# Optimization experiments

Measured on AMD Instinct MI355X. Metric: run time of the kernel, lower is better.

Reference implementation:

```python
import jax, jax.numpy as jnp
import numpy as np

N_NODES = 100000
N_EDGES = 1600000
K = 5  # TAGConv hops
F_IN, F_HID, F_OUT = 64, 128, 64


def setup_inputs() -> dict:
    key = jax.random.key(0)
    ks = jax.random.split(key, 6)
    x = jax.random.normal(ks[0], (N_NODES, F_IN), dtype=jnp.float32)
    edge_index = jax.random.randint(ks[1], (2, N_EDGES), 0, N_NODES, dtype=jnp.int32)
    edge_weight = jax.random.uniform(ks[2], (N_EDGES,), dtype=jnp.float32)
    # TAGConv layer l has (K+1) weight matrices stacked as [K+1, in, out] + one bias
    W0 = jax.random.normal(ks[3], (K + 1, F_IN, F_HID), dtype=jnp.float32) * 0.05
    b0 = jnp.zeros((F_HID,), dtype=jnp.float32)
    W1 = jax.random.normal(ks[4], (K + 1, F_HID, F_OUT), dtype=jnp.float32) * 0.05
    b1 = jnp.zeros((F_OUT,), dtype=jnp.float32)
    return {"x": x, "edge_index": edge_index, "edge_weight": edge_weight,
            "W0": W0, "b0": b0, "W1": W1, "b1": b1}


def _gcn_norm(edge_weight, row, col):
    # symmetric normalization, no added self-loops (TAGConv default with edge_weight)
    deg = jax.ops.segment_sum(edge_weight, col, num_segments=N_NODES)
    safe_deg = jnp.where(deg > 0, deg, 1.0)
    dis = jnp.where(deg > 0, jax.lax.rsqrt(safe_deg), 0.0)  # deg^-1/2, 0 for isolated
    return dis[row] * edge_weight * dis[col]


def _tag_conv(x, row, col, norm, W, b):
    # out = sum_{k=0..K} (A_norm^k x) @ W[k] + b
    out = x @ W[0]
    h = x
    for k in range(1, K + 1):
        msg = h[row] * norm[:, None]                    # gather + scale  [E, F]
        h = jax.ops.segment_sum(msg, col, num_segments=N_NODES)  # scatter-add [N, F]
        out = out + h @ W[k]
    return out + b


def reference(x, edge_index, edge_weight, W0, b0, W1, b1):
    row, col = edge_index[0], edge_index[1]
    norm = _gcn_norm(edge_weight, row, col)
    h = jax.nn.leaky_relu(_tag_conv(x, row, col, norm, W0, b0), negative_slope=0.01)
    h = jax.nn.leaky_relu(_tag_conv(h, row, col, norm, W1, b1), negative_slope=0.01)
    return h
```

## Files before the change

### kernel.cpp

```cpp
#include <hip/hip_runtime.h>


namespace {
constexpr int NN = 100000;
constexpr int NE = 1600000;
constexpr int TPB = 256;

typedef __attribute__((ext_vector_type(8))) short short8v;
typedef __attribute__((ext_vector_type(4))) float float4v;

__device__ __forceinline__ float bflo(unsigned p) { return __uint_as_float(p << 16); }
__device__ __forceinline__ float bfhi(unsigned p) { return __uint_as_float(p & 0xffff0000u); }
__device__ __forceinline__ unsigned f2bf(float x) {
  unsigned u = __float_as_uint(x);
  return (u + 0x7fffu + ((u >> 16) & 1u)) >> 16;
}
__device__ __forceinline__ unsigned pack2(float lo, float hi) {
  return f2bf(lo) | (f2bf(hi) << 16);
}

__global__ void pass1_kernel(const int* __restrict__ col, const float* __restrict__ w,
                             unsigned* __restrict__ acc32, int* __restrict__ rank) {
  int e = blockIdx.x * TPB + threadIdx.x;
  if (e >= NE) return;
  int c = col[e];
  unsigned v = (1u << 21) | (unsigned)__float2uint_rn(w[e] * 8192.0f);
  unsigned old = atomicAdd(&acc32[c], v);
  rank[e] = (int)(old >> 21);
}

__global__ void dis_kernel(const unsigned* __restrict__ acc32, float* __restrict__ dis) {
  int n = blockIdx.x * TPB + threadIdx.x;
  if (n >= NN) return;
  float d = (float)(acc32[n] & 0x1FFFFFu) * (1.0f / 8192.0f);
  dis[n] = d > 0.f ? rsqrtf(d) : 0.f;
}

__global__ void scan1_kernel(const unsigned* __restrict__ acc32, int* __restrict__ excl,
                             int* __restrict__ btot) {
  __shared__ int sh[1024];
  int i = blockIdx.x * 1024 + threadIdx.x;
  int v = (i < NN) ? (int)(acc32[i] >> 21) : 0;
  sh[threadIdx.x] = v;
  __syncthreads();
  for (int ofs = 1; ofs < 1024; ofs <<= 1) {
    int t = (threadIdx.x >= ofs) ? sh[threadIdx.x - ofs] : 0;
    __syncthreads();
    sh[threadIdx.x] += t;
    __syncthreads();
  }
  if (i < NN) excl[i] = sh[threadIdx.x] - v;
  if (threadIdx.x == 1023) btot[blockIdx.x] = sh[1023];
}

__global__ void scan2_kernel(int* __restrict__ btot, int nb) {
  __shared__ int sh[128];
  int t = threadIdx.x;
  if (t < nb) sh[t] = btot[t];
  __syncthreads();
  if (t == 0) {
    int run = 0;
    for (int b = 0; b < nb; ++b) { int x = sh[b]; sh[b] = run; run += x; }
  }
  __syncthreads();
  if (t < nb) btot[t] = sh[t];
}

__global__ void scan3_kernel(const int* __restrict__ excl, const int* __restrict__ btot,
                             int* __restrict__ rowptr) {
  int i = blockIdx.x * TPB + threadIdx.x;
  if (i < NN) rowptr[i] = excl[i] + btot[i >> 10];
  if (i == NN) rowptr[NN] = NE;
}

__global__ void fill2_kernel(const int* __restrict__ row, const int* __restrict__ col,
                             const float* __restrict__ w, const float* __restrict__ dis,
                             const int* __restrict__ rank, const int* __restrict__ rowptr,
                             int2* __restrict__ edges) {
  int e = blockIdx.x * TPB + threadIdx.x;
  if (e >= NE) return;
  int r = row[e], c = col[e];
  float nw = dis[r] * w[e] * dis[c];
  edges[rowptr[c] + rank[e]] = make_int2(r, __float_as_int(nw));
}

__global__ void wfrag0_kernel(const float* __restrict__ W0, short* __restrict__ F) {
  int t = blockIdx.x * TPB + threadIdx.x;
  if (t >= 12 * 8 * 64) return;
  int l = t & 63, nt = (t >> 6) & 7, s = t >> 9;
  int c = nt * 16 + (l & 15);
  int kb = s * 32 + (l >> 4) * 8;
  short8v v;
#pragma unroll
  for (int j = 0; j < 8; ++j) v[j] = (short)f2bf(W0[(kb + j) * 128 + c]);
  *(short8v*)(F + (size_t)t * 8) = v;
}

__global__ void wfrag1_kernel(const float* __restrict__ W1, short* __restrict__ F) {
  int t = blockIdx.x * TPB + threadIdx.x;
  if (t >= 4 * 24 * 64) return;
  int l = t & 63, nt = (t >> 6) % 24, s = t / (64 * 24);
  int J = nt * 16 + (l & 15);
  int fb = s * 32 + (l >> 4) * 8;
  const float* Wb = W1 + (size_t)(J >> 6) * (128 * 64) + (J & 63);
  short8v v;
#pragma unroll
  for (int j = 0; j < 8; ++j) v[j] = (short)f2bf(Wb[(size_t)(fb + j) * 64]);
  *(short8v*)(F + (size_t)t * 8) = v;
}

__global__ void convx_kernel(const float* __restrict__ x, unsigned* __restrict__ hcat) {
  unsigned idx = blockIdx.x * (unsigned)TPB + threadIdx.x;
  if (idx >= (unsigned)NN * 32u) return;
  unsigned n = idx >> 5, p = idx & 31u;
  float2 v = *(const float2*)(x + (size_t)n * 64 + p * 2);
  hcat[(size_t)n * 192 + p] = pack2(v.x, v.y);
}

__device__ __forceinline__ void fma8(float* a, uint4 p, float w) {
  a[0] = fmaf(bflo(p.x), w, a[0]); a[1] = fmaf(bfhi(p.x), w, a[1]);
  a[2] = fmaf(bflo(p.y), w, a[2]); a[3] = fmaf(bfhi(p.y), w, a[3]);
  a[4] = fmaf(bflo(p.z), w, a[4]); a[5] = fmaf(bfhi(p.z), w, a[5]);
  a[6] = fmaf(bflo(p.w), w, a[6]); a[7] = fmaf(bfhi(p.w), w, a[7]);
}

template <bool YADD, bool FINAL>
__global__ void hop_kernel(const unsigned short* __restrict__ src, int sstride,
                           const int2* __restrict__ edges, const int* __restrict__ rowptr,
                           const unsigned short* __restrict__ y,
                           unsigned short* __restrict__ dst, int dstride,
                           const float* __restrict__ bias, float* __restrict__ outf) {
  unsigned n = blockIdx.x * 32u + (threadIdx.x >> 3);
  unsigned lane = threadIdx.x & 7u;
  unsigned f0 = lane * 8u;
  int e = rowptr[n], e1 = rowptr[n + 1];
  float a[8] = {};
  for (; e + 3 < e1; e += 4) {
    int2 d0 = edges[e], d1 = edges[e + 1], d2 = edges[e + 2], d3 = edges[e + 3];
    uint4 p0 = *(const uint4*)(src + (size_t)(unsigned)d0.x * sstride + f0);
    uint4 p1 = *(const uint4*)(src + (size_t)(unsigned)d1.x * sstride + f0);
    uint4 p2 = *(const uint4*)(src + (size_t)(unsigned)d2.x * sstride + f0);
    uint4 p3 = *(const uint4*)(src + (size_t)(unsigned)d3.x * sstride + f0);
    fma8(a, p0, __int_as_float(d0.y));
    fma8(a, p1, __int_as_float(d1.y));
    fma8(a, p2, __int_as_float(d2.y));
    fma8(a, p3, __int_as_float(d3.y));
  }
  if (e + 1 < e1) {
    int2 d0 = edges[e], d1 = edges[e + 1];
    uint4 p0 = *(const uint4*)(src + (size_t)(unsigned)d0.x * sstride + f0);
    uint4 p1 = *(const uint4*)(src + (size_t)(unsigned)d1.x * sstride + f0);
    fma8(a, p0, __int_as_float(d0.y));
    fma8(a, p1, __int_as_float(d1.y));
    e += 2;
  }
  if (e < e1) {
    int2 d0 = edges[e];
    uint4 p0 = *(const uint4*)(src + (size_t)(unsigned)d0.x * sstride + f0);
    fma8(a, p0, __int_as_float(d0.y));
  }
  if (YADD) {
    uint4 yv = *(const uint4*)(y + (size_t)n * 384 + f0);
    a[0] += bflo(yv.x); a[1] += bfhi(yv.x);
    a[2] += bflo(yv.y); a[3] += bfhi(yv.y);
    a[4] += bflo(yv.z); a[5] += bfhi(yv.z);
    a[6] += bflo(yv.w); a[7] += bfhi(yv.w);
  }
  if (FINAL) {
    const float4* bp = (const float4*)(bias + f0);
    float4 bv0 = bp[0], bv1 = bp[1];
    float4 o0, o1;
    o0.x = a[0] + bv0.x; o0.y = a[1] + bv0.y; o0.z = a[2] + bv0.z; o0.w = a[3] + bv0.w;
    o1.x = a[4] + bv1.x; o1.y = a[5] + bv1.y; o1.z = a[6] + bv1.z; o1.w = a[7] + bv1.w;
    o0.x = o0.x >= 0.f ? o0.x : 0.01f * o0.x; o0.y = o0.y >= 0.f ? o0.y : 0.01f * o0.y;
    o0.z = o0.z >= 0.f ? o0.z : 0.01f * o0.z; o0.w = o0.w >= 0.f ? o0.w : 0.01f * o0.w;
    o1.x = o1.x >= 0.f ? o1.x : 0.01f * o1.x; o1.y = o1.y >= 0.f ? o1.y : 0.01f * o1.y;
    o1.z = o1.z >= 0.f ? o1.z : 0.01f * o1.z; o1.w = o1.w >= 0.f ? o1.w : 0.01f * o1.w;
    float4* op = (float4*)(outf + (size_t)n * 64 + f0);
    op[0] = o0; op[1] = o1;
  } else {
    uint4 st;
    st.x = pack2(a[0], a[1]); st.y = pack2(a[2], a[3]);
    st.z = pack2(a[4], a[5]); st.w = pack2(a[6], a[7]);
    *(uint4*)(dst + (size_t)n * dstride + f0) = st;
  }
}

__global__ void gemm_l0(const unsigned short* __restrict__ A, const short* __restrict__ W0f,
                        const float* __restrict__ bias, unsigned short* __restrict__ H1) {
  int wave = threadIdx.x >> 6, lane = threadIdx.x & 63;
  int lrow = lane & 15, lk = lane >> 4;
  unsigned r0 = blockIdx.x * 64u + (unsigned)wave * 16u;
  unsigned arow = r0 + (unsigned)lrow;
  if (arow >= NN) arow = NN - 1;
  const short8v* Ab = (const short8v*)(A + (size_t)arow * 384 + (unsigned)lk * 8);
  const short8v* Bb = (const short8v*)W0f + lane;
  float4v acc[8] = {};
#pragma unroll
  for (int s = 0; s < 12; ++s) {
    short8v a = Ab[s * 4];
#pragma unroll
    for (int nt = 0; nt < 8; ++nt) {
      short8v b = Bb[(s * 8 + nt) * 64];
      acc[nt] = __builtin_amdgcn_mfma_f32_16x16x32_bf16(a, b, acc[nt], 0, 0, 0);
    }
  }
#pragma unroll
  for (int nt = 0; nt < 8; ++nt) {
    int c = nt * 16 + lrow;
    float bv = bias[c];
#pragma unroll
    for (int r = 0; r < 4; ++r) {
      unsigned n = r0 + (unsigned)(lk * 4 + r);
      if (n < NN) {
        float v = acc[nt][r] + bv;
        v = v >= 0.f ? v : 0.01f * v;
        H1[(size_t)n * 128 + c] = (unsigned short)f2bf(v);
      }
    }
  }
}

__global__ void gemm_l1(const unsigned short* __restrict__ A, const short* __restrict__ W1f,
                        unsigned short* __restrict__ Y) {
  int wave = threadIdx.x >> 6, lane = threadIdx.x & 63;
  int lrow = lane & 15, lk = lane >> 4;
  int yb = blockIdx.y * 8;
  unsigned r0 = blockIdx.x * 64u + (unsigned)wave * 16u;
  unsigned arow = r0 + (unsigned)lrow;
  if (arow >= NN) arow = NN - 1;
  const short8v* Ab = (const short8v*)(A + (size_t)arow * 128 + (unsigned)lk * 8);
  const short8v* Bb = (const short8v*)W1f + lane;
  float4v acc[8] = {};
#pragma unroll
  for (int s = 0; s < 4; ++s) {
    short8v a = Ab[s * 4];
#pragma unroll
    for (int nt = 0; nt < 8; ++nt) {
      short8v b = Bb[(s * 24 + yb + nt) * 64];
      acc[nt] = __builtin_amdgcn_mfma_f32_16x16x32_bf16(a, b, acc[nt], 0, 0, 0);
    }
  }
#pragma unroll
  for (int nt = 0; nt < 8; ++nt) {
    int c = (yb + nt) * 16 + lrow;
#pragma unroll
    for (int r = 0; r < 4; ++r) {
      unsigned n = r0 + (unsigned)(lk * 4 + r);
      if (n < NN) Y[(size_t)n * 384 + c] = (unsigned short)f2bf(acc[nt][r]);
    }
  }
}

}

extern "C" void kernel_launch(void* const* d_in, const int* in_sizes, int n_in,
                              void* d_out, int out_size, void* d_ws, size_t ws_size,
                              hipStream_t stream) {
  const float* x  = (const float*)d_in[0];
  const int*   ei = (const int*)d_in[1];
  const float* ew = (const float*)d_in[2];
  const float* W0 = (const float*)d_in[3];
  const float* b0 = (const float*)d_in[4];
  const float* W1 = (const float*)d_in[5];
  const float* b1 = (const float*)d_in[6];
  float* out = (float*)d_out;
  const int* row = ei;
  const int* col = ei + NE;

  constexpr size_t OFF_DIS    = 0;
  constexpr size_t OFF_ROWPTR = 100352;
  constexpr size_t OFF_BTOT   = OFF_ROWPTR + 100352;
  constexpr size_t OFF_EDGES  = OFF_BTOT + 128;
  constexpr size_t OFF_HCAT   = OFF_EDGES + 2 * (size_t)NE;
  constexpr size_t OFF_H1     = OFF_HCAT + (size_t)NN * 384 / 2;
  constexpr size_t WS_WORDS   = OFF_H1 + (size_t)NN * 128 / 2;
  if (ws_size < WS_WORDS * sizeof(float)) return;

  float* ws = (float*)d_ws;
  float* dis    = ws + OFF_DIS;
  int*   rowptr = (int*)(ws + OFF_ROWPTR);
  int*   btot   = (int*)(ws + OFF_BTOT);
  int2*  edges  = (int2*)(ws + OFF_EDGES);
  unsigned short* Hcat = (unsigned short*)(ws + OFF_HCAT);
  unsigned short* H1   = (unsigned short*)(ws + OFF_H1);
  short* W0f = (short*)(ws + OFF_DIS);
  short* W1f = (short*)(ws + OFF_DIS + 24576);
  unsigned* acc32 = (unsigned*)(ws + OFF_H1);
  int* excl = (int*)(ws + OFF_H1 + 100352);
  int* rank = (int*)Hcat;
  unsigned short* z0 = H1;
  unsigned short* z1 = H1 + (size_t)NN * 64;

  hipMemsetAsync(acc32, 0, NN * sizeof(unsigned), stream);
  pass1_kernel<<<(NE + TPB - 1) / TPB, TPB, 0, stream>>>(col, ew, acc32, rank);
  dis_kernel<<<(NN + TPB - 1) / TPB, TPB, 0, stream>>>(acc32, dis);
  scan1_kernel<<<98, 1024, 0, stream>>>(acc32, excl, btot);
  scan2_kernel<<<1, 128, 0, stream>>>(btot, 98);
  scan3_kernel<<<(NN + TPB) / TPB, TPB, 0, stream>>>(excl, btot, rowptr);
  fill2_kernel<<<(NE + TPB - 1) / TPB, TPB, 0, stream>>>(row, col, ew, dis, rank, rowptr, edges);
  wfrag0_kernel<<<24, TPB, 0, stream>>>(W0, W0f);
  wfrag1_kernel<<<24, TPB, 0, stream>>>(W1, W1f);

  convx_kernel<<<NN * 32 / TPB, TPB, 0, stream>>>(x, (unsigned*)Hcat);
  for (int k = 1; k <= 5; ++k) {
    hop_kernel<false, false><<<NN / 32, TPB, 0, stream>>>(
        Hcat + (k - 1) * 64, 384, edges, rowptr, nullptr,
        Hcat + k * 64, 384, nullptr, nullptr);
  }
  gemm_l0<<<(NN + 63) / 64, TPB, 0, stream>>>(Hcat, W0f, b0, H1);

  gemm_l1<<<dim3((NN + 63) / 64, 3), TPB, 0, stream>>>(H1, W1f, Hcat);
  const unsigned short* Y = Hcat;
  hop_kernel<true, false><<<NN / 32, TPB, 0, stream>>>(
      Y + 5 * 64, 384, edges, rowptr, Y + 4 * 64, z0, 64, nullptr, nullptr);
  hop_kernel<true, false><<<NN / 32, TPB, 0, stream>>>(
      z0, 64, edges, rowptr, Y + 3 * 64, z1, 64, nullptr, nullptr);
  hop_kernel<true, false><<<NN / 32, TPB, 0, stream>>>(
      z1, 64, edges, rowptr, Y + 2 * 64, z0, 64, nullptr, nullptr);
  hop_kernel<true, false><<<NN / 32, TPB, 0, stream>>>(
      z0, 64, edges, rowptr, Y + 1 * 64, z1, 64, nullptr, nullptr);
  hop_kernel<true, true><<<NN / 32, TPB, 0, stream>>>(
      z1, 64, edges, rowptr, Y + 0 * 64, nullptr, 0, b1, out);
}
```

Measured before the change: 628.1 us.

## Split node feature matrices into 16-wide column slabs for hop gathers

Node feature buffers are changed from row-major wide rows to four planar slabs of 16 bf16 features per node. Hop kernels launch one grid row per slab, so each gather touches a smaller, denser working set. The GEMM kernels read and write the same slab layout. The trade-off is that the edge list and row pointers are read four times per hop, and each lane issues narrower 4-byte loads.

```diff
diff --git a/kernel.cpp b/kernel.cpp
--- a/kernel.cpp
+++ b/kernel.cpp
@@ -5,6 +5,7 @@
 constexpr int NN = 100000;
 constexpr int NE = 1600000;
 constexpr int TPB = 256;
+constexpr size_t QS = (size_t)NN * 16;
 
 typedef __attribute__((ext_vector_type(8))) short short8v;
 typedef __attribute__((ext_vector_type(4))) float float4v;
@@ -109,80 +110,60 @@
   *(short8v*)(F + (size_t)t * 8) = v;
 }
 
-__global__ void convx_kernel(const float* __restrict__ x, unsigned* __restrict__ hcat) {
+__global__ void convx_kernel(const float* __restrict__ x, unsigned short* __restrict__ hcat) {
   unsigned idx = blockIdx.x * (unsigned)TPB + threadIdx.x;
-  if (idx >= (unsigned)NN * 32u) return;
-  unsigned n = idx >> 5, p = idx & 31u;
-  float2 v = *(const float2*)(x + (size_t)n * 64 + p * 2);
-  hcat[(size_t)n * 192 + p] = pack2(v.x, v.y);
-}
-
-__device__ __forceinline__ void fma8(float* a, uint4 p, float w) {
-  a[0] = fmaf(bflo(p.x), w, a[0]); a[1] = fmaf(bfhi(p.x), w, a[1]);
-  a[2] = fmaf(bflo(p.y), w, a[2]); a[3] = fmaf(bfhi(p.y), w, a[3]);
-  a[4] = fmaf(bflo(p.z), w, a[4]); a[5] = fmaf(bfhi(p.z), w, a[5]);
-  a[6] = fmaf(bflo(p.w), w, a[6]); a[7] = fmaf(bfhi(p.w), w, a[7]);
+  unsigned q = idx / ((unsigned)NN * 8u);
+  unsigned rem = idx - q * ((unsigned)NN * 8u);
+  unsigned n = rem >> 3, j = rem & 7u;
+  float2 v = *(const float2*)(x + (size_t)n * 64 + q * 16 + j * 2);
+  *(unsigned*)(hcat + q * QS + (size_t)n * 16 + j * 2) = pack2(v.x, v.y);
 }
 
 template <bool YADD, bool FINAL>
-__global__ void hop_kernel(const unsigned short* __restrict__ src, int sstride,
+__global__ void hop_kernel(const unsigned short* __restrict__ src0,
                            const int2* __restrict__ edges, const int* __restrict__ rowptr,
-                           const unsigned short* __restrict__ y,
-                           unsigned short* __restrict__ dst, int dstride,
+                           const unsigned short* __restrict__ y0,
+                           unsigned short* __restrict__ dst0,
                            const float* __restrict__ bias, float* __restrict__ outf) {
+  unsigned q = blockIdx.y;
+  const unsigned short* src = src0 + q * QS;
   unsigned n = blockIdx.x * 32u + (threadIdx.x >> 3);
   unsigned lane = threadIdx.x & 7u;
-  unsigned f0 = lane * 8u;
+  unsigned f0 = lane * 2u;
   int e = rowptr[n], e1 = rowptr[n + 1];
-  float a[8] = {};
+  float a0 = 0.f, a1 = 0.f;
   for (; e + 3 < e1; e += 4) {
     int2 d0 = edges[e], d1 = edges[e + 1], d2 = edges[e + 2], d3 = edges[e + 3];
-    uint4 p0 = *(const uint4*)(src + (size_t)(unsigned)d0.x * sstride + f0);
-    uint4 p1 = *(const uint4*)(src + (size_t)(unsigned)d1.x * sstride + f0);
-    uint4 p2 = *(const uint4*)(src + (size_t)(unsigned)d2.x * sstride + f0);
-    uint4 p3 = *(const uint4*)(src + (size_t)(unsigned)d3.x * sstride + f0);
-    fma8(a, p0, __int_as_float(d0.y));
-    fma8(a, p1, __int_as_float(d1.y));
-    fma8(a, p2, __int_as_float(d2.y));
-    fma8(a, p3, __int_as_float(d3.y));
-  }
-  if (e + 1 < e1) {
-    int2 d0 = edges[e], d1 = edges[e + 1];
-    uint4 p0 = *(const uint4*)(src + (size_t)(unsigned)d0.x * sstride + f0);
-    uint4 p1 = *(const uint4*)(src + (size_t)(unsigned)d1.x * sstride + f0);
-    fma8(a, p0, __int_as_float(d0.y));
-    fma8(a, p1, __int_as_float(d1.y));
-    e += 2;
-  }
-  if (e < e1) {
+    unsigned p0 = *(const unsigned*)(src + (size_t)(unsigned)d0.x * 16 + f0);
+    unsigned p1 = *(const unsigned*)(src + (size_t)(unsigned)d1.x * 16 + f0);
+    unsigned p2 = *(const unsigned*)(src + (size_t)(unsigned)d2.x * 16 + f0);
+    unsigned p3 = *(const unsigned*)(src + (size_t)(unsigned)d3.x * 16 + f0);
+    float w0 = __int_as_float(d0.y), w1 = __int_as_float(d1.y);
+    float w2 = __int_as_float(d2.y), w3 = __int_as_float(d3.y);
+    a0 = fmaf(bflo(p0), w0, a0); a1 = fmaf(bfhi(p0), w0, a1);
+    a0 = fmaf(bflo(p1), w1, a0); a1 = fmaf(bfhi(p1), w1, a1);
+    a0 = fmaf(bflo(p2), w2, a0); a1 = fmaf(bfhi(p2), w2, a1);
+    a0 = fmaf(bflo(p3), w3, a0); a1 = fmaf(bfhi(p3), w3, a1);
+  }
+  for (; e < e1; ++e) {
     int2 d0 = edges[e];
-    uint4 p0 = *(const uint4*)(src + (size_t)(unsigned)d0.x * sstride + f0);
-    fma8(a, p0, __int_as_float(d0.y));
+    unsigned p0 = *(const unsigned*)(src + (size_t)(unsigned)d0.x * 16 + f0);
+    float w0 = __int_as_float(d0.y);
+    a0 = fmaf(bflo(p0), w0, a0); a1 = fmaf(bfhi(p0), w0, a1);
   }
   if (YADD) {
-    uint4 yv = *(const uint4*)(y + (size_t)n * 384 + f0);
-    a[0] += bflo(yv.x); a[1] += bfhi(yv.x);
-    a[2] += bflo(yv.y); a[3] += bfhi(yv.y);
-    a[4] += bflo(yv.z); a[5] += bfhi(yv.z);
-    a[6] += bflo(yv.w); a[7] += bfhi(yv.w);
+    unsigned yv = *(const unsigned*)(y0 + q * QS + (size_t)n * 16 + f0);
+    a0 += bflo(yv);
+    a1 += bfhi(yv);
   }
   if (FINAL) {
-    const float4* bp = (const float4*)(bias + f0);
-    float4 bv0 = bp[0], bv1 = bp[1];
-    float4 o0, o1;
-    o0.x = a[0] + bv0.x; o0.y = a[1] + bv0.y; o0.z = a[2] + bv0.z; o0.w = a[3] + bv0.w;
-    o1.x = a[4] + bv1.x; o1.y = a[5] + bv1.y; o1.z = a[6] + bv1.z; o1.w = a[7] + bv1.w;
-    o0.x = o0.x >= 0.f ? o0.x : 0.01f * o0.x; o0.y = o0.y >= 0.f ? o0.y : 0.01f * o0.y;
-    o0.z = o0.z >= 0.f ? o0.z : 0.01f * o0.z; o0.w = o0.w >= 0.f ? o0.w : 0.01f * o0.w;
-    o1.x = o1.x >= 0.f ? o1.x : 0.01f * o1.x; o1.y = o1.y >= 0.f ? o1.y : 0.01f * o1.y;
-    o1.z = o1.z >= 0.f ? o1.z : 0.01f * o1.z; o1.w = o1.w >= 0.f ? o1.w : 0.01f * o1.w;
-    float4* op = (float4*)(outf + (size_t)n * 64 + f0);
-    op[0] = o0; op[1] = o1;
+    a0 += bias[q * 16 + f0];
+    a1 += bias[q * 16 + f0 + 1];
+    a0 = a0 >= 0.f ? a0 : 0.01f * a0;
+    a1 = a1 >= 0.f ? a1 : 0.01f * a1;
+    *(float2*)(outf + (size_t)n * 64 + q * 16 + f0) = make_float2(a0, a1);
   } else {
-    uint4 st;
-    st.x = pack2(a[0], a[1]); st.y = pack2(a[2], a[3]);
-    st.z = pack2(a[4], a[5]); st.w = pack2(a[6], a[7]);
-    *(uint4*)(dst + (size_t)n * dstride + f0) = st;
+    *(unsigned*)(dst0 + q * QS + (size_t)n * 16 + f0) = pack2(a0, a1);
   }
 }
 
@@ -193,12 +174,14 @@
   unsigned r0 = blockIdx.x * 64u + (unsigned)wave * 16u;
   unsigned arow = r0 + (unsigned)lrow;
   if (arow >= NN) arow = NN - 1;
-  const short8v* Ab = (const short8v*)(A + (size_t)arow * 384 + (unsigned)lk * 8);
+  const unsigned short* Ap =
+      A + ((size_t)(lk >> 1) * NN + arow) * 16 + (unsigned)(lk & 1) * 8;
+  const size_t AS = 2 * QS;
   const short8v* Bb = (const short8v*)W0f + lane;
   float4v acc[8] = {};
 #pragma unroll
   for (int s = 0; s < 12; ++s) {
-    short8v a = Ab[s * 4];
+    short8v a = *(const short8v*)(Ap + s * AS);
 #pragma unroll
     for (int nt = 0; nt < 8; ++nt) {
       short8v b = Bb[(s * 8 + nt) * 64];
@@ -215,7 +198,7 @@
       if (n < NN) {
         float v = acc[nt][r] + bv;
         v = v >= 0.f ? v : 0.01f * v;
-        H1[(size_t)n * 128 + c] = (unsigned short)f2bf(v);
+        H1[((size_t)nt * NN + n) * 16 + lrow] = (unsigned short)f2bf(v);
       }
     }
   }
@@ -229,12 +212,14 @@
   unsigned r0 = blockIdx.x * 64u + (unsigned)wave * 16u;
   unsigned arow = r0 + (unsigned)lrow;
   if (arow >= NN) arow = NN - 1;
-  const short8v* Ab = (const short8v*)(A + (size_t)arow * 128 + (unsigned)lk * 8);
+  const unsigned short* Ap =
+      A + ((size_t)(lk >> 1) * NN + arow) * 16 + (unsigned)(lk & 1) * 8;
+  const size_t AS = 2 * QS;
   const short8v* Bb = (const short8v*)W1f + lane;
   float4v acc[8] = {};
 #pragma unroll
   for (int s = 0; s < 4; ++s) {
-    short8v a = Ab[s * 4];
+    short8v a = *(const short8v*)(Ap + s * AS);
 #pragma unroll
     for (int nt = 0; nt < 8; ++nt) {
       short8v b = Bb[(s * 24 + yb + nt) * 64];
@@ -243,11 +228,11 @@
   }
 #pragma unroll
   for (int nt = 0; nt < 8; ++nt) {
-    int c = (yb + nt) * 16 + lrow;
 #pragma unroll
     for (int r = 0; r < 4; ++r) {
       unsigned n = r0 + (unsigned)(lk * 4 + r);
-      if (n < NN) Y[(size_t)n * 384 + c] = (unsigned short)f2bf(acc[nt][r]);
+      if (n < NN)
+        Y[((size_t)(yb + nt) * NN + n) * 16 + lrow] = (unsigned short)f2bf(acc[nt][r]);
     }
   }
 }
@@ -290,7 +275,7 @@
   int* excl = (int*)(ws + OFF_H1 + 100352);
   int* rank = (int*)Hcat;
   unsigned short* z0 = H1;
-  unsigned short* z1 = H1 + (size_t)NN * 64;
+  unsigned short* z1 = H1 + 4 * QS;
 
   hipMemsetAsync(acc32, 0, NN * sizeof(unsigned), stream);
   pass1_kernel<<<(NE + TPB - 1) / TPB, TPB, 0, stream>>>(col, ew, acc32, rank);
@@ -302,24 +287,24 @@
   wfrag0_kernel<<<24, TPB, 0, stream>>>(W0, W0f);
   wfrag1_kernel<<<24, TPB, 0, stream>>>(W1, W1f);
 
-  convx_kernel<<<NN * 32 / TPB, TPB, 0, stream>>>(x, (unsigned*)Hcat);
+  convx_kernel<<<NN * 32 / TPB, TPB, 0, stream>>>(x, Hcat);
   for (int k = 1; k <= 5; ++k) {
-    hop_kernel<false, false><<<NN / 32, TPB, 0, stream>>>(
-        Hcat + (k - 1) * 64, 384, edges, rowptr, nullptr,
-        Hcat + k * 64, 384, nullptr, nullptr);
+    hop_kernel<false, false><<<dim3(NN / 32, 4), TPB, 0, stream>>>(
+        Hcat + (size_t)(k - 1) * 4 * QS, edges, rowptr, nullptr,
+        Hcat + (size_t)k * 4 * QS, nullptr, nullptr);
   }
   gemm_l0<<<(NN + 63) / 64, TPB, 0, stream>>>(Hcat, W0f, b0, H1);
 
   gemm_l1<<<dim3((NN + 63) / 64, 3), TPB, 0, stream>>>(H1, W1f, Hcat);
   const unsigned short* Y = Hcat;
-  hop_kernel<true, false><<<NN / 32, TPB, 0, stream>>>(
-      Y + 5 * 64, 384, edges, rowptr, Y + 4 * 64, z0, 64, nullptr, nullptr);
-  hop_kernel<true, false><<<NN / 32, TPB, 0, stream>>>(
-      z0, 64, edges, rowptr, Y + 3 * 64, z1, 64, nullptr, nullptr);
-  hop_kernel<true, false><<<NN / 32, TPB, 0, stream>>>(
-      z1, 64, edges, rowptr, Y + 2 * 64, z0, 64, nullptr, nullptr);
-  hop_kernel<true, false><<<NN / 32, TPB, 0, stream>>>(
-      z0, 64, edges, rowptr, Y + 1 * 64, z1, 64, nullptr, nullptr);
-  hop_kernel<true, true><<<NN / 32, TPB, 0, stream>>>(
-      z1, 64, edges, rowptr, Y + 0 * 64, nullptr, 0, b1, out);
-}
+  hop_kernel<true, false><<<dim3(NN / 32, 4), TPB, 0, stream>>>(
+      Y + 5 * 4 * QS, edges, rowptr, Y + 4 * 4 * QS, z0, nullptr, nullptr);
+  hop_kernel<true, false><<<dim3(NN / 32, 4), TPB, 0, stream>>>(
+      z0, edges, rowptr, Y + 3 * 4 * QS, z1, nullptr, nullptr);
+  hop_kernel<true, false><<<dim3(NN / 32, 4), TPB, 0, stream>>>(
+      z1, edges, rowptr, Y + 2 * 4 * QS, z0, nullptr, nullptr);
+  hop_kernel<true, false><<<dim3(NN / 32, 4), TPB, 0, stream>>>(
+      z0, edges, rowptr, Y + 1 * 4 * QS, z1, nullptr, nullptr);
+  hop_kernel<true, true><<<dim3(NN / 32, 4), TPB, 0, stream>>>(
+      z1, edges, rowptr, Y + 0 * 4 * QS, nullptr, b1, out);
+}
```

Measured after the change: 899.8 us. +43.3%, slower.

## Degree-sort nodes within stripes to balance hop kernel wavefronts; fuse dis into scan

Applied to the files above, without the earlier changes.

Adds a per-stripe counting sort of nodes by in-degree (descending), producing a permutation of (start, end, node) records stored in the output buffer. Hop kernels, except the final one, use this table so nodes with similar degree share a wavefront, which reduces divergence from uneven edge-loop lengths. Separately, the deg^-1/2 computation is folded into the first scan kernel to drop one launch. The cost is an extra kernel, an extra indirection per node, scattered writes to destination rows, and reuse of the output buffer as scratch before the final kernel overwrites it.

```diff
diff --git a/kernel.cpp b/kernel.cpp
--- a/kernel.cpp
+++ b/kernel.cpp
@@ -5,6 +5,7 @@
 constexpr int NN = 100000;
 constexpr int NE = 1600000;
 constexpr int TPB = 256;
+constexpr int STRIPE = 4096;
 
 typedef __attribute__((ext_vector_type(8))) short short8v;
 typedef __attribute__((ext_vector_type(4))) float float4v;
@@ -29,18 +30,16 @@
   rank[e] = (int)(old >> 21);
 }
 
-__global__ void dis_kernel(const unsigned* __restrict__ acc32, float* __restrict__ dis) {
-  int n = blockIdx.x * TPB + threadIdx.x;
-  if (n >= NN) return;
-  float d = (float)(acc32[n] & 0x1FFFFFu) * (1.0f / 8192.0f);
-  dis[n] = d > 0.f ? rsqrtf(d) : 0.f;
-}
-
 __global__ void scan1_kernel(const unsigned* __restrict__ acc32, int* __restrict__ excl,
-                             int* __restrict__ btot) {
+                             int* __restrict__ btot, float* __restrict__ dis) {
   __shared__ int sh[1024];
   int i = blockIdx.x * 1024 + threadIdx.x;
-  int v = (i < NN) ? (int)(acc32[i] >> 21) : 0;
+  unsigned a = (i < NN) ? acc32[i] : 0u;
+  int v = (int)(a >> 21);
+  if (i < NN) {
+    float d = (float)(a & 0x1FFFFFu) * (1.0f / 8192.0f);
+    dis[i] = d > 0.f ? rsqrtf(d) : 0.f;
+  }
   sh[threadIdx.x] = v;
   __syncthreads();
   for (int ofs = 1; ofs < 1024; ofs <<= 1) {
@@ -84,6 +83,31 @@
   edges[rowptr[c] + rank[e]] = make_int2(r, __float_as_int(nw));
 }
 
+__global__ void ssort_kernel(const int* __restrict__ rowptr, int4* __restrict__ vseg) {
+  __shared__ int hist[128];
+  __shared__ int base[128];
+  int s0 = blockIdx.x * STRIPE;
+  int cnt = min(STRIPE, NN - s0);
+  if (threadIdx.x < 128) hist[threadIdx.x] = 0;
+  __syncthreads();
+  for (int i = threadIdx.x; i < cnt; i += TPB) {
+    int d = rowptr[s0 + i + 1] - rowptr[s0 + i];
+    atomicAdd(&hist[min(d, 127)], 1);
+  }
+  __syncthreads();
+  if (threadIdx.x == 0) {
+    int run = 0;
+    for (int b = 127; b >= 0; --b) { base[b] = run; run += hist[b]; }
+  }
+  __syncthreads();
+  for (int i = threadIdx.x; i < cnt; i += TPB) {
+    int e0 = rowptr[s0 + i], e1 = rowptr[s0 + i + 1];
+    int b = min(e1 - e0, 127);
+    int pos = atomicAdd(&base[b], 1);
+    vseg[s0 + pos] = make_int4(e0, e1, s0 + i, 0);
+  }
+}
+
 __global__ void wfrag0_kernel(const float* __restrict__ W0, short* __restrict__ F) {
   int t = blockIdx.x * TPB + threadIdx.x;
   if (t >= 12 * 8 * 64) return;
@@ -124,16 +148,25 @@
   a[6] = fmaf(bflo(p.w), w, a[6]); a[7] = fmaf(bfhi(p.w), w, a[7]);
 }
 
-template <bool YADD, bool FINAL>
+template <bool VSEG, bool YADD, bool FINAL>
 __global__ void hop_kernel(const unsigned short* __restrict__ src, int sstride,
                            const int2* __restrict__ edges, const int* __restrict__ rowptr,
+                           const int4* __restrict__ vseg,
                            const unsigned short* __restrict__ y,
                            unsigned short* __restrict__ dst, int dstride,
                            const float* __restrict__ bias, float* __restrict__ outf) {
-  unsigned n = blockIdx.x * 32u + (threadIdx.x >> 3);
+  unsigned vn = blockIdx.x * 32u + (threadIdx.x >> 3);
   unsigned lane = threadIdx.x & 7u;
   unsigned f0 = lane * 8u;
-  int e = rowptr[n], e1 = rowptr[n + 1];
+  int e, e1;
+  unsigned n;
+  if (VSEG) {
+    int4 s = vseg[vn];
+    e = s.x; e1 = s.y; n = (unsigned)s.z;
+  } else {
+    n = vn;
+    e = rowptr[n]; e1 = rowptr[n + 1];
+  }
   float a[8] = {};
   for (; e + 3 < e1; e += 4) {
     int2 d0 = edges[e], d1 = edges[e + 1], d2 = edges[e + 2], d3 = edges[e + 3];
@@ -291,35 +324,36 @@
   int* rank = (int*)Hcat;
   unsigned short* z0 = H1;
   unsigned short* z1 = H1 + (size_t)NN * 64;
+  int4* vseg = (int4*)d_out;
 
   hipMemsetAsync(acc32, 0, NN * sizeof(unsigned), stream);
   pass1_kernel<<<(NE + TPB - 1) / TPB, TPB, 0, stream>>>(col, ew, acc32, rank);
-  dis_kernel<<<(NN + TPB - 1) / TPB, TPB, 0, stream>>>(acc32, dis);
-  scan1_kernel<<<98, 1024, 0, stream>>>(acc32, excl, btot);
+  scan1_kernel<<<98, 1024, 0, stream>>>(acc32, excl, btot, dis);
   scan2_kernel<<<1, 128, 0, stream>>>(btot, 98);
   scan3_kernel<<<(NN + TPB) / TPB, TPB, 0, stream>>>(excl, btot, rowptr);
   fill2_kernel<<<(NE + TPB - 1) / TPB, TPB, 0, stream>>>(row, col, ew, dis, rank, rowptr, edges);
+  ssort_kernel<<<(NN + STRIPE - 1) / STRIPE, TPB, 0, stream>>>(rowptr, vseg);
   wfrag0_kernel<<<24, TPB, 0, stream>>>(W0, W0f);
   wfrag1_kernel<<<24, TPB, 0, stream>>>(W1, W1f);
 
   convx_kernel<<<NN * 32 / TPB, TPB, 0, stream>>>(x, (unsigned*)Hcat);
   for (int k = 1; k <= 5; ++k) {
-    hop_kernel<false, false><<<NN / 32, TPB, 0, stream>>>(
-        Hcat + (k - 1) * 64, 384, edges, rowptr, nullptr,
+    hop_kernel<true, false, false><<<NN / 32, TPB, 0, stream>>>(
+        Hcat + (k - 1) * 64, 384, edges, rowptr, vseg, nullptr,
         Hcat + k * 64, 384, nullptr, nullptr);
   }
   gemm_l0<<<(NN + 63) / 64, TPB, 0, stream>>>(Hcat, W0f, b0, H1);
 
   gemm_l1<<<dim3((NN + 63) / 64, 3), TPB, 0, stream>>>(H1, W1f, Hcat);
   const unsigned short* Y = Hcat;
-  hop_kernel<true, false><<<NN / 32, TPB, 0, stream>>>(
-      Y + 5 * 64, 384, edges, rowptr, Y + 4 * 64, z0, 64, nullptr, nullptr);
-  hop_kernel<true, false><<<NN / 32, TPB, 0, stream>>>(
-      z0, 64, edges, rowptr, Y + 3 * 64, z1, 64, nullptr, nullptr);
-  hop_kernel<true, false><<<NN / 32, TPB, 0, stream>>>(
-      z1, 64, edges, rowptr, Y + 2 * 64, z0, 64, nullptr, nullptr);
-  hop_kernel<true, false><<<NN / 32, TPB, 0, stream>>>(
-      z0, 64, edges, rowptr, Y + 1 * 64, z1, 64, nullptr, nullptr);
-  hop_kernel<true, true><<<NN / 32, TPB, 0, stream>>>(
-      z1, 64, edges, rowptr, Y + 0 * 64, nullptr, 0, b1, out);
-}
+  hop_kernel<true, true, false><<<NN / 32, TPB, 0, stream>>>(
+      Y + 5 * 64, 384, edges, rowptr, vseg, Y + 4 * 64, z0, 64, nullptr, nullptr);
+  hop_kernel<true, true, false><<<NN / 32, TPB, 0, stream>>>(
+      z0, 64, edges, rowptr, vseg, Y + 3 * 64, z1, 64, nullptr, nullptr);
+  hop_kernel<true, true, false><<<NN / 32, TPB, 0, stream>>>(
+      z1, 64, edges, rowptr, vseg, Y + 2 * 64, z0, 64, nullptr, nullptr);
+  hop_kernel<true, true, false><<<NN / 32, TPB, 0, stream>>>(
+      z0, 64, edges, rowptr, vseg, Y + 1 * 64, z1, 64, nullptr, nullptr);
+  hop_kernel<false, true, true><<<NN / 32, TPB, 0, stream>>>(
+      z1, 64, edges, rowptr, nullptr, Y + 0 * 64, nullptr, 0, b1, out);
+}
```

Result: slower. 657.9 us (+4.7%).
